# Kernel tuning notes

Measured on AMD Instinct MI355X. Metric: run time of the kernel, lower is better.

The kernel has to match this reference:

```python
import jax, jax.numpy as jnp
import numpy as np

EPS = 1e-08


def setup_inputs() -> dict:
    key = jax.random.key(0)
    k_x, k_w1, k_b1, k_w2, k_b2 = jax.random.split(key, 5)
    B, C, T = 64, 64, 4000
    x = jax.random.normal(k_x, (B, C, T, 1), dtype=jnp.float32)
    # 1x1 Conv2D with in_channels=1, out_channels=8 -> weight is an 8-vector + bias
    w1 = jax.random.normal(k_w1, (8,), dtype=jnp.float32) * 0.5
    b1 = jax.random.normal(k_b1, (8,), dtype=jnp.float32) * 0.1
    w2 = jax.random.normal(k_w2, (8,), dtype=jnp.float32) * 0.5
    b2 = jax.random.normal(k_b2, (8,), dtype=jnp.float32) * 0.1
    # gamma is initialized to 0 in the module (residual identity at init);
    # use a nonzero value so the attention path is exercised numerically.
    gamma = jnp.float32(0.5)
    return {"x": x, "w1": w1, "b1": b1, "w2": w2, "b2": b2, "gamma": gamma}


def reference(x, w1, b1, w2, b2, gamma):
    B, C, T, _ = x.shape  # (B, num_ch, T, 1)
    # 1x1 conv with C_in=1: broadcast multiply-add, then flatten (T, 8) -> T*8
    q = (x * w1 + b1).reshape(B, C, T * 8)  # proj_query (B, C, T*8)
    k = (x * w2 + b2).reshape(B, C, T * 8)  # proj_key   (B, C, T*8)
    # energy = Q @ K^T  -> (B, C, C)
    energy = jnp.einsum('bcd,bed->bce', q, k)
    # custom min-max normalization along last axis, then softmax
    max_h = jnp.max(energy, axis=2, keepdims=True)
    min_h = jnp.min(energy, axis=2, keepdims=True)
    energy = (energy - min_h) / (max_h - min_h + EPS)
    attention = jax.nn.softmax(energy, axis=-1)
    xs = x[..., 0]  # squeeze last dim -> (B, C, T)
    # attention^T @ xs  (transpose_a=True)
    attended = jnp.einsum('bec,bet->bct', attention, xs)
    return gamma * attended[..., None] + x
```

## Files before the change

kernel.cpp:

```cpp
#include <hip/hip_runtime.h>

#define BB 64
#define CC 64
#define TT 4000

#define SLABS 16
#define TSLAB 250
#define GP_PITCH 264

#define TPB 128
#define NT2 ((TT + TPB - 1) / TPB)
#define XPITCH 132
#define APITCH 72

#define GPART_ELEMS ((size_t)SLABS * BB * CC * CC)
#define SPART_ELEMS ((size_t)SLABS * BB * CC)

typedef short short8 __attribute__((ext_vector_type(8)));
typedef float f32x16 __attribute__((ext_vector_type(16)));

__device__ __forceinline__ short f2bf(float f) {
    unsigned u = __float_as_uint(f);
    u = (u + 0x7FFFu + ((u >> 16) & 1u)) >> 16;
    return (short)u;
}
__device__ __forceinline__ float bfpair(unsigned u) {
    return __uint_as_float(u << 16) + __uint_as_float(u & 0xFFFF0000u);
}

__global__ __launch_bounds__(256)
void gram_mfma(const float* __restrict__ x, float* __restrict__ G_part,
               float* __restrict__ S_part) {
    __shared__ short xs[CC * GP_PITCH];
    __shared__ float sred[4 * 64];
    const int b    = blockIdx.x / SLABS;
    const int slab = blockIdx.x % SLABS;
    const int t0   = slab * TSLAB;
    const int tid  = threadIdx.x;
    const int lane = tid & 63;
    const int wave = tid >> 6;
    const float* xb = x + (size_t)b * CC * TT;

    for (int i = tid; i < 64 * 64; i += 256) {
        int row = i >> 6, tq = i & 63;
        float4 v = make_float4(0.f, 0.f, 0.f, 0.f);
        if (tq < 62) {
            v = *(const float4*)(xb + row * TT + t0 + 4 * tq);
        } else if (tq == 62) {
            const float* p = xb + row * TT + t0 + 248;
            v.x = p[0]; v.y = p[1];
        }
        short4 sv;
        sv.x = f2bf(v.x); sv.y = f2bf(v.y); sv.z = f2bf(v.z); sv.w = f2bf(v.w);
        int pc = (tq >> 1) ^ (row & 7);
        *(short4*)(xs + row * GP_PITCH + pc * 8 + (tq & 1) * 4) = sv;
    }
    __syncthreads();

    {
        const short* rowp = xs + lane * GP_PITCH;
        float s = 0.f;
        #pragma unroll
        for (int j = 0; j < 8; ++j) {
            int pc = (wave * 8 + j) ^ (lane & 7);
            uint2 u0 = *(const uint2*)(rowp + pc * 8);
            uint2 u1 = *(const uint2*)(rowp + pc * 8 + 4);
            s += bfpair(u0.x) + bfpair(u0.y) + bfpair(u1.x) + bfpair(u1.y);
        }
        sred[wave * 64 + lane] = s;
    }
    __syncthreads();
    if (tid < 64) {
        float s = sred[tid] + sred[64 + tid] + sred[128 + tid] + sred[192 + tid];
        S_part[(slab * BB + b) * CC + tid] = s;
    }

    const int r0 = (wave >> 1) * 32, c0 = (wave & 1) * 32;
    const int m = lane & 31, half = lane >> 5;
    f32x16 acc;
    #pragma unroll
    for (int z = 0; z < 16; ++z) acc[z] = 0.f;
    #pragma unroll
    for (int ks = 0; ks < 16; ++ks) {
        const int ck = ks * 2 + half;
        short8 av = *(const short8*)(xs + (r0 + m) * GP_PITCH + (ck ^ (m & 7)) * 8);
        short8 bv = *(const short8*)(xs + (c0 + m) * GP_PITCH + (ck ^ (m & 7)) * 8);
        acc = __builtin_amdgcn_mfma_f32_32x32x16_bf16(av, bv, acc, 0, 0, 0);
    }
    float* gp = G_part + ((size_t)slab * BB + b) * (CC * CC);
    #pragma unroll
    for (int r = 0; r < 16; ++r) {
        const int row = (r & 3) + 8 * (r >> 2) + 4 * half;
        gp[(r0 + row) * CC + (c0 + m)] = acc[r];
    }
}

__global__ __launch_bounds__(256)
void softmax_fused(const float* __restrict__ w1, const float* __restrict__ b1,
                   const float* __restrict__ w2, const float* __restrict__ b2,
                   const float* __restrict__ G_part, const float* __restrict__ S_part,
                   float* __restrict__ attG) {
    __shared__ float Es[64 * 65];
    __shared__ float Sb[64];
    __shared__ float red_mn[4 * 64], red_mx[4 * 64], red_sm[4 * 64];
    const int b   = blockIdx.x;
    const int tid = threadIdx.x;
    const int c = tid & 63, q = tid >> 6;

    for (int j = tid; j < 4096; j += 256) {
        float s = 0.f;
        #pragma unroll
        for (int sl = 0; sl < SLABS; ++sl)
            s += G_part[((size_t)sl * BB + b) * 4096 + j];
        Es[(j >> 6) * 65 + (j & 63)] = s;
    }
    if (tid < 64) {
        float s = 0.f;
        #pragma unroll
        for (int sl = 0; sl < SLABS; ++sl)
            s += S_part[(sl * BB + b) * CC + tid];
        Sb[tid] = s;
    }
    float A = 0.f, Bc = 0.f, Be = 0.f, Cc = 0.f;
    #pragma unroll
    for (int j = 0; j < 8; ++j) {
        float a1 = w1[j], a2 = w2[j], q1 = b1[j], q2 = b2[j];
        A += a1 * a2; Bc += a1 * q2; Be += q1 * a2; Cc += q1 * q2;
    }
    Cc *= (float)TT;
    __syncthreads();

    const float sc = Sb[c];
    float ev[16], mn = 1e30f, mx = -1e30f;
    #pragma unroll
    for (int i = 0; i < 16; ++i) {
        const int e = 16 * q + i;
        float en = A * Es[c * 65 + e] + Bc * sc + Be * Sb[e] + Cc;
        ev[i] = en;
        mn = fminf(mn, en); mx = fmaxf(mx, en);
    }
    red_mn[q * 64 + c] = mn; red_mx[q * 64 + c] = mx;
    __syncthreads();
    mn = fminf(fminf(red_mn[c], red_mn[64 + c]), fminf(red_mn[128 + c], red_mn[192 + c]));
    mx = fmaxf(fmaxf(red_mx[c], red_mx[64 + c]), fmaxf(red_mx[128 + c], red_mx[192 + c]));
    const float ninv = 1.f / (mx - mn + 1e-8f);
    float pv[16], ls = 0.f;
    #pragma unroll
    for (int i = 0; i < 16; ++i) {
        float p = __expf((ev[i] - mn) * ninv);
        pv[i] = p; ls += p;
    }
    red_sm[q * 64 + c] = ls;
    __syncthreads();
    const float rinv = 1.f / (red_sm[c] + red_sm[64 + c] + red_sm[128 + c] + red_sm[192 + c]);
    #pragma unroll
    for (int i = 0; i < 16; ++i) Es[c * 65 + 16 * q + i] = pv[i] * rinv;
    __syncthreads();
    float* ab = attG + (size_t)b * 4096;
    for (int j = tid; j < 4096; j += 256) {
        int cc = j >> 6, ee = j & 63;
        ab[j] = Es[ee * 65 + cc];
    }
}

__global__ __launch_bounds__(256)
void apply_mfma(const float* __restrict__ x, const float* __restrict__ attG,
                const float* __restrict__ gamma, float* __restrict__ out) {
    __shared__ float xs[CC * XPITCH];
    __shared__ short al[CC * APITCH];
    const int b  = blockIdx.x / NT2;
    const int t0 = (blockIdx.x % NT2) * TPB;
    const int tid = threadIdx.x;
    const int lane = tid & 63, wave = tid >> 6;
    const float* xb = x + (size_t)b * CC * TT;
    const float* ab = attG + (size_t)b * CC * CC;

    for (int i = tid; i < CC * (TPB / 4); i += 256) {
        int e = i >> 5, p = i & 31;
        int t = t0 + 4 * p;
        float4 v = make_float4(0.f, 0.f, 0.f, 0.f);
        if (t < TT) v = *(const float4*)(xb + e * TT + t);
        *(float4*)(xs + e * XPITCH + 4 * p) = v;
    }
    for (int i = tid; i < CC * CC / 4; i += 256) {
        int c = i >> 4, qq = i & 15;
        float4 v = *(const float4*)(ab + c * CC + 4 * qq);
        short4 sv;
        sv.x = f2bf(v.x); sv.y = f2bf(v.y); sv.z = f2bf(v.z); sv.w = f2bf(v.w);
        *(short4*)(al + c * APITCH + 4 * qq) = sv;
    }
    __syncthreads();

    const int m = lane & 31, half = lane >> 5;
    const int c0 = (wave & 1) * 32;
    const int tb = (wave >> 1) * 64;
    f32x16 acc0, acc1;
    #pragma unroll
    for (int z = 0; z < 16; ++z) { acc0[z] = 0.f; acc1[z] = 0.f; }

    #pragma unroll
    for (int ks = 0; ks < 4; ++ks) {
        short8 av = *(const short8*)(al + (c0 + m) * APITCH + ks * 16 + 8 * half);
        const int eb = ks * 16 + 8 * half;
        short8 bv0, bv1;
        #pragma unroll
        for (int j = 0; j < 8; ++j) {
            bv0[j] = f2bf(xs[(eb + j) * XPITCH + tb + m]);
            bv1[j] = f2bf(xs[(eb + j) * XPITCH + tb + 32 + m]);
        }
        acc0 = __builtin_amdgcn_mfma_f32_32x32x16_bf16(av, bv0, acc0, 0, 0, 0);
        acc1 = __builtin_amdgcn_mfma_f32_32x32x16_bf16(av, bv1, acc1, 0, 0, 0);
    }

    const float gm = gamma[0];
    float* ob = out + (size_t)b * CC * TT;
    #pragma unroll
    for (int r = 0; r < 16; ++r) {
        const int row = (r & 3) + 8 * (r >> 2) + 4 * half;
        const int c = c0 + row;
        const int tl0 = tb + m, tl1 = tb + 32 + m;
        const int tg0 = t0 + tl0, tg1 = t0 + tl1;
        if (tg0 < TT) ob[c * TT + tg0] = gm * acc0[r] + xs[c * XPITCH + tl0];
        if (tg1 < TT) ob[c * TT + tg1] = gm * acc1[r] + xs[c * XPITCH + tl1];
    }
}

extern "C" void kernel_launch(void* const* d_in, const int* in_sizes, int n_in,
                              void* d_out, int out_size, void* d_ws, size_t ws_size,
                              hipStream_t stream) {
    const float* x  = (const float*)d_in[0];
    const float* w1 = (const float*)d_in[1];
    const float* b1 = (const float*)d_in[2];
    const float* w2 = (const float*)d_in[3];
    const float* b2 = (const float*)d_in[4];
    const float* gm = (const float*)d_in[5];
    float* out = (float*)d_out;

    float* G_part = (float*)d_ws;
    float* S_part = G_part + GPART_ELEMS;
    float* attG   = S_part + SPART_ELEMS;

    hipLaunchKernelGGL(gram_mfma, dim3(BB * SLABS), dim3(256), 0, stream,
                       x, G_part, S_part);
    hipLaunchKernelGGL(softmax_fused, dim3(BB), dim3(256), 0, stream,
                       w1, b1, w2, b2, G_part, S_part, attG);
    hipLaunchKernelGGL(apply_mfma, dim3(BB * NT2), dim3(256), 0, stream,
                       x, attG, gm, out);
}
```

Measured before the change: 167.2 us.

## Split softmax across row groups and store x tile as transposed bf16

The softmax kernel now runs 8 blocks per batch instead of one. Each wave handles one row, reducing the slab partials and doing min/max/sum with wave shuffles instead of shared-memory reductions. The apply kernel converts x to bf16 once while staging it into a transposed, XOR-swizzled shared tile, so MFMA B operands are vector loads rather than per-element converts. The residual add now re-reads x from global memory instead of shared memory, which adds some global traffic but halves the shared tile size.

After: 167.5 us. About the same (+0.2%).

```diff
diff --git a/kernel.cpp b/kernel.cpp
--- a/kernel.cpp
+++ b/kernel.cpp
@@ -10,7 +10,7 @@
 
 #define TPB 128
 #define NT2 ((TT + TPB - 1) / TPB)
-#define XPITCH 132
+#define XTP 72
 #define APITCH 72
 
 #define GPART_ELEMS ((size_t)SLABS * BB * CC * CC)
@@ -96,24 +96,16 @@
 }
 
 __global__ __launch_bounds__(256)
-void softmax_fused(const float* __restrict__ w1, const float* __restrict__ b1,
+void softmax_split(const float* __restrict__ w1, const float* __restrict__ b1,
                    const float* __restrict__ w2, const float* __restrict__ b2,
                    const float* __restrict__ G_part, const float* __restrict__ S_part,
                    float* __restrict__ attG) {
-    __shared__ float Es[64 * 65];
     __shared__ float Sb[64];
-    __shared__ float red_mn[4 * 64], red_mx[4 * 64], red_sm[4 * 64];
-    const int b   = blockIdx.x;
+    __shared__ float Pt[64 * 12];
+    const int b = blockIdx.x >> 3, g = blockIdx.x & 7;
     const int tid = threadIdx.x;
-    const int c = tid & 63, q = tid >> 6;
-
-    for (int j = tid; j < 4096; j += 256) {
-        float s = 0.f;
-        #pragma unroll
-        for (int sl = 0; sl < SLABS; ++sl)
-            s += G_part[((size_t)sl * BB + b) * 4096 + j];
-        Es[(j >> 6) * 65 + (j & 63)] = s;
-    }
+    const int lane = tid & 63, w = tid >> 6;
+
     if (tid < 64) {
         float s = 0.f;
         #pragma unroll
@@ -130,43 +122,40 @@
     Cc *= (float)TT;
     __syncthreads();
 
-    const float sc = Sb[c];
-    float ev[16], mn = 1e30f, mx = -1e30f;
-    #pragma unroll
-    for (int i = 0; i < 16; ++i) {
-        const int e = 16 * q + i;
-        float en = A * Es[c * 65 + e] + Bc * sc + Be * Sb[e] + Cc;
-        ev[i] = en;
-        mn = fminf(mn, en); mx = fmaxf(mx, en);
-    }
-    red_mn[q * 64 + c] = mn; red_mx[q * 64 + c] = mx;
-    __syncthreads();
-    mn = fminf(fminf(red_mn[c], red_mn[64 + c]), fminf(red_mn[128 + c], red_mn[192 + c]));
-    mx = fmaxf(fmaxf(red_mx[c], red_mx[64 + c]), fmaxf(red_mx[128 + c], red_mx[192 + c]));
-    const float ninv = 1.f / (mx - mn + 1e-8f);
-    float pv[16], ls = 0.f;
-    #pragma unroll
-    for (int i = 0; i < 16; ++i) {
-        float p = __expf((ev[i] - mn) * ninv);
-        pv[i] = p; ls += p;
-    }
-    red_sm[q * 64 + c] = ls;
-    __syncthreads();
-    const float rinv = 1.f / (red_sm[c] + red_sm[64 + c] + red_sm[128 + c] + red_sm[192 + c]);
-    #pragma unroll
-    for (int i = 0; i < 16; ++i) Es[c * 65 + 16 * q + i] = pv[i] * rinv;
+    #pragma unroll
+    for (int pass = 0; pass < 2; ++pass) {
+        const int rl = 4 * pass + w;
+        const int r  = 8 * g + rl;
+        float v = 0.f;
+        #pragma unroll
+        for (int sl = 0; sl < SLABS; ++sl)
+            v += G_part[(((size_t)sl * BB + b) << 12) + r * 64 + lane];
+        float en = A * v + Bc * Sb[r] + Be * Sb[lane] + Cc;
+        float mx = en, mn = en;
+        #pragma unroll
+        for (int off = 32; off; off >>= 1) {
+            mx = fmaxf(mx, __shfl_xor(mx, off, 64));
+            mn = fminf(mn, __shfl_xor(mn, off, 64));
+        }
+        float p = __expf((en - mn) / (mx - mn + 1e-8f));
+        float sum = p;
+        #pragma unroll
+        for (int off = 32; off; off >>= 1) sum += __shfl_xor(sum, off, 64);
+        Pt[lane * 12 + rl] = p / sum;
+    }
     __syncthreads();
     float* ab = attG + (size_t)b * 4096;
-    for (int j = tid; j < 4096; j += 256) {
-        int cc = j >> 6, ee = j & 63;
-        ab[j] = Es[ee * 65 + cc];
+    if (tid < 128) {
+        int c = tid >> 1, h = tid & 1;
+        float4 v = *(const float4*)(Pt + c * 12 + 4 * h);
+        *(float4*)(ab + c * 64 + 8 * g + 4 * h) = v;
     }
 }
 
 __global__ __launch_bounds__(256)
 void apply_mfma(const float* __restrict__ x, const float* __restrict__ attG,
                 const float* __restrict__ gamma, float* __restrict__ out) {
-    __shared__ float xs[CC * XPITCH];
+    __shared__ short xt[TPB * XTP];
     __shared__ short al[CC * APITCH];
     const int b  = blockIdx.x / NT2;
     const int t0 = (blockIdx.x % NT2) * TPB;
@@ -175,25 +164,46 @@
     const float* xb = x + (size_t)b * CC * TT;
     const float* ab = attG + (size_t)b * CC * CC;
 
-    for (int i = tid; i < CC * (TPB / 4); i += 256) {
-        int e = i >> 5, p = i & 31;
-        int t = t0 + 4 * p;
-        float4 v = make_float4(0.f, 0.f, 0.f, 0.f);
-        if (t < TT) v = *(const float4*)(xb + e * TT + t);
-        *(float4*)(xs + e * XPITCH + 4 * p) = v;
-    }
     for (int i = tid; i < CC * CC / 4; i += 256) {
-        int c = i >> 4, qq = i & 15;
-        float4 v = *(const float4*)(ab + c * CC + 4 * qq);
+        int c = i >> 4, q = i & 15;
+        float4 v = *(const float4*)(ab + c * CC + 4 * q);
         short4 sv;
         sv.x = f2bf(v.x); sv.y = f2bf(v.y); sv.z = f2bf(v.z); sv.w = f2bf(v.w);
-        *(short4*)(al + c * APITCH + 4 * qq) = sv;
+        *(short4*)(al + c * APITCH + 4 * q) = sv;
+    }
+    #pragma unroll
+    for (int it = 0; it < 2; ++it) {
+        const int tg = tid & 31;
+        const int eg = (tid >> 5) + 8 * it;
+        const int e0 = 4 * eg;
+        const int tl = 4 * tg;
+        const int t  = t0 + tl;
+        float4 v0, v1, v2, v3;
+        if (t < TT) {
+            v0 = *(const float4*)(xb + (e0 + 0) * TT + t);
+            v1 = *(const float4*)(xb + (e0 + 1) * TT + t);
+            v2 = *(const float4*)(xb + (e0 + 2) * TT + t);
+            v3 = *(const float4*)(xb + (e0 + 3) * TT + t);
+        } else {
+            v0 = v1 = v2 = v3 = make_float4(0.f, 0.f, 0.f, 0.f);
+        }
+        #pragma unroll
+        for (int j = 0; j < 4; ++j) {
+            float a = (j == 0) ? v0.x : (j == 1) ? v0.y : (j == 2) ? v0.z : v0.w;
+            float bq = (j == 0) ? v1.x : (j == 1) ? v1.y : (j == 2) ? v1.z : v1.w;
+            float cq = (j == 0) ? v2.x : (j == 1) ? v2.y : (j == 2) ? v2.z : v2.w;
+            float dq = (j == 0) ? v3.x : (j == 1) ? v3.y : (j == 2) ? v3.z : v3.w;
+            short4 sv; sv.x = f2bf(a); sv.y = f2bf(bq); sv.z = f2bf(cq); sv.w = f2bf(dq);
+            int pc = eg ^ ((tl + j) & 15);
+            *(short4*)(xt + (tl + j) * XTP + 4 * pc) = sv;
+        }
     }
     __syncthreads();
 
     const int m = lane & 31, half = lane >> 5;
     const int c0 = (wave & 1) * 32;
     const int tb = (wave >> 1) * 64;
+    const int s0 = (tb + m) & 15;
     f32x16 acc0, acc1;
     #pragma unroll
     for (int z = 0; z < 16; ++z) { acc0[z] = 0.f; acc1[z] = 0.f; }
@@ -201,27 +211,29 @@
     #pragma unroll
     for (int ks = 0; ks < 4; ++ks) {
         short8 av = *(const short8*)(al + (c0 + m) * APITCH + ks * 16 + 8 * half);
-        const int eb = ks * 16 + 8 * half;
-        short8 bv0, bv1;
-        #pragma unroll
-        for (int j = 0; j < 8; ++j) {
-            bv0[j] = f2bf(xs[(eb + j) * XPITCH + tb + m]);
-            bv1[j] = f2bf(xs[(eb + j) * XPITCH + tb + 32 + m]);
-        }
+        const int lc = 4 * ks + 2 * half;
+        const int p0 = lc ^ s0, p1 = p0 ^ 1;
+        const short* r0p = xt + (tb + m) * XTP;
+        const short* r1p = xt + (tb + 32 + m) * XTP;
+        short4 b0l = *(const short4*)(r0p + 4 * p0);
+        short4 b0h = *(const short4*)(r0p + 4 * p1);
+        short4 b1l = *(const short4*)(r1p + 4 * p0);
+        short4 b1h = *(const short4*)(r1p + 4 * p1);
+        short8 bv0 = {b0l.x, b0l.y, b0l.z, b0l.w, b0h.x, b0h.y, b0h.z, b0h.w};
+        short8 bv1 = {b1l.x, b1l.y, b1l.z, b1l.w, b1h.x, b1h.y, b1h.z, b1h.w};
         acc0 = __builtin_amdgcn_mfma_f32_32x32x16_bf16(av, bv0, acc0, 0, 0, 0);
         acc1 = __builtin_amdgcn_mfma_f32_32x32x16_bf16(av, bv1, acc1, 0, 0, 0);
     }
 
     const float gm = gamma[0];
     float* ob = out + (size_t)b * CC * TT;
+    const int tg0 = t0 + tb + m, tg1 = tg0 + 32;
     #pragma unroll
     for (int r = 0; r < 16; ++r) {
         const int row = (r & 3) + 8 * (r >> 2) + 4 * half;
         const int c = c0 + row;
-        const int tl0 = tb + m, tl1 = tb + 32 + m;
-        const int tg0 = t0 + tl0, tg1 = t0 + tl1;
-        if (tg0 < TT) ob[c * TT + tg0] = gm * acc0[r] + xs[c * XPITCH + tl0];
-        if (tg1 < TT) ob[c * TT + tg1] = gm * acc1[r] + xs[c * XPITCH + tl1];
+        if (tg0 < TT) ob[c * TT + tg0] = gm * acc0[r] + xb[c * TT + tg0];
+        if (tg1 < TT) ob[c * TT + tg1] = gm * acc1[r] + xb[c * TT + tg1];
     }
 }
 
@@ -242,7 +254,7 @@
 
     hipLaunchKernelGGL(gram_mfma, dim3(BB * SLABS), dim3(256), 0, stream,
                        x, G_part, S_part);
-    hipLaunchKernelGGL(softmax_fused, dim3(BB), dim3(256), 0, stream,
+    hipLaunchKernelGGL(softmax_split, dim3(BB * 8), dim3(256), 0, stream,
                        w1, b1, w2, b2, G_part, S_part, attG);
     hipLaunchKernelGGL(apply_mfma, dim3(BB * NT2), dim3(256), 0, stream,
                        x, attG, gm, out);
```
